# Optimization experiments

Hardware: AMD Instinct MI355X
Metric: run time of the kernel (lower is better)

The kernel has to match this reference:

```python
import jax, jax.numpy as jnp
import numpy as np

B, N, DIM = 4, 2048, 512
HEADS, DK = 8, 64
SCALE = DK ** -0.5


def setup_inputs() -> dict:
    key = jax.random.key(0)
    k1, k2, k3, k4 = jax.random.split(key, 4)
    x = jax.random.normal(k1, (B, N, DIM), dtype=jnp.float32)
    # nn.Linear(dim, dim_key*heads, bias=False): y = x @ W.T; store W already transposed
    Wq = jax.random.normal(k2, (DIM, HEADS * DK), dtype=jnp.float32) * (DIM ** -0.5)
    Wk = jax.random.normal(k3, (DIM, HEADS * DK), dtype=jnp.float32) * (DIM ** -0.5)
    rel_content_bias = jax.random.normal(k4, (1, HEADS, 1, DK), dtype=jnp.float32)
    return {"x": x, "Wq": Wq, "Wk": Wk, "rel_content_bias": rel_content_bias}


def _split_heads(t, h):
    # [b, n, h*d] -> [b, h, n, d]
    b, n, hd = t.shape
    return t.reshape(b, n, h, hd // h).transpose(0, 2, 1, 3)


def reference(x, Wq, Wk, rel_content_bias):
    q = _split_heads(x @ Wq, HEADS) * SCALE          # [b, h, n, dk]
    k = _split_heads(x @ Wk, HEADS)                  # [b, h, n, dk]
    v = _split_heads(x, HEADS)                       # [b, h, n, dim/h]
    logits = jnp.einsum('bhid,bhjd->bhij', q + rel_content_bias, k)
    attn = jax.nn.sigmoid(logits)                    # no softmax normalization
    out = jnp.einsum('bhij,bhjd->bhid', attn, v)     # [b, h, n, dim/h]
    b, h, n, d = out.shape
    return out.transpose(0, 2, 1, 3).reshape(b, n, h * d)
```

## Files before the change

kernel.cpp:

```cpp
#include <hip/hip_runtime.h>
#include <hip/hip_bf16.h>
#include <stdint.h>

#define BB 4
#define NN 2048
#define DIMD 512
#define HH 8
#define DKK 64
#define MTOT (BB * NN)
constexpr float SCALE = 0.125f;
constexpr float L2E = 1.44269504089f;

typedef __attribute__((ext_vector_type(4))) float f32x4;
typedef __attribute__((ext_vector_type(2))) float f32x2;
typedef __attribute__((ext_vector_type(8))) short bf16x8;
typedef __attribute__((ext_vector_type(4))) _Float16 f16x4;
typedef __attribute__((ext_vector_type(2))) __fp16 fp16v2;
typedef __attribute__((ext_vector_type(4))) __fp16 fp16v4;
typedef __attribute__((ext_vector_type(2))) unsigned int u32x2;

union pack8 { unsigned short s[8]; uint4 v; };
union fragu { u32x2 h[2]; bf16x8 v; };

__device__ __forceinline__ unsigned short f2bf(float f) {
  union { float f; uint32_t u; } v; v.f = f;
  uint32_t u = v.u;
  return (unsigned short)((u + 0x7FFFu + ((u >> 16) & 1u)) >> 16);
}

__device__ __forceinline__ unsigned short f2h(float f) {
  union { _Float16 h; unsigned short u; } c; c.h = (_Float16)f;
  return c.u;
}

__device__ __forceinline__ bf16x8 ld_frag(const unsigned short* p) {
  fragu f;
  f.h[0] = *(const u32x2*)p;
  f.h[1] = *(const u32x2*)(p + 4);
  return f.v;
}
__device__ __forceinline__ void st8(unsigned short* p, uint4 v) {
  *(u32x2*)p = (u32x2){v.x, v.y};
  *(u32x2*)(p + 4) = (u32x2){v.z, v.w};
}

__device__ __forceinline__ f16x4 sig_pack(f32x4 sv) {
  float e0 = __builtin_amdgcn_exp2f(-__builtin_fabsf(sv[0]));
  float e1 = __builtin_amdgcn_exp2f(-__builtin_fabsf(sv[1]));
  float e2 = __builtin_amdgcn_exp2f(-__builtin_fabsf(sv[2]));
  float e3 = __builtin_amdgcn_exp2f(-__builtin_fabsf(sv[3]));
  const f32x2 c3 = {-0.22184f, -0.22184f};
  const f32x2 c2 = {0.66550f, 0.66550f};
  const f32x2 c1 = {-0.94280f, -0.94280f};
  const f32x2 c0 = {0.49826f, 0.49826f};
  f32x2 eA = {e0, e1}, eB = {e2, e3};
  f32x2 pA = __builtin_elementwise_fma(
      __builtin_elementwise_fma(__builtin_elementwise_fma(c3, eA, c2), eA, c1),
      eA, c0);
  f32x2 pB = __builtin_elementwise_fma(
      __builtin_elementwise_fma(__builtin_elementwise_fma(c3, eB, c2), eB, c1),
      eB, c0);
  float r0 = __builtin_copysignf(pA.x, sv[0]);
  float r1 = __builtin_copysignf(pA.y, sv[1]);
  float r2 = __builtin_copysignf(pB.x, sv[2]);
  float r3 = __builtin_copysignf(pB.y, sv[3]);
  fp16v2 lo = __builtin_amdgcn_cvt_pkrtz(r0, r1);
  fp16v2 hi = __builtin_amdgcn_cvt_pkrtz(r2, r3);
  fp16v4 p;
  p.x = lo.x; p.y = lo.y; p.z = hi.x; p.w = hi.y;
  return __builtin_bit_cast(f16x4, p);
}

__global__ __launch_bounds__(256) void prep(const float* __restrict__ x,
                                            const float* __restrict__ wq,
                                            const float* __restrict__ wk,
                                            unsigned short* __restrict__ xtf,
                                            unsigned short* __restrict__ wtq,
                                            unsigned short* __restrict__ wtk,
                                            float* __restrict__ vsum_p) {
  const int bx = blockIdx.x, tid = threadIdx.x;
  if (bx < 256) {
    __shared__ float Pred[4][64];
    int q = bx;
    int b = q >> 6, r = q & 63;
    int dt = r >> 3, nt = r & 7;
    int dl = tid & 63, c = tid >> 6;
    int d = dt * 64 + dl;
    int n0 = nt * 256 + c * 64;
    const float* xp = x + ((size_t)b * NN + n0) * DIMD + d;
    unsigned short* dp = xtf + ((size_t)b * DIMD + d) * NN + n0;
    float s = 0.f;
#pragma unroll
    for (int g = 0; g < 8; g++) {
      pack8 pa;
#pragma unroll
      for (int k = 0; k < 8; k++) {
        float v = xp[(size_t)(g * 8 + k) * DIMD];
        s += v;
        pa.s[k] = f2h(v);
      }
      *(uint4*)(dp + g * 8) = pa.v;
    }
    Pred[c][dl] = s;
    __syncthreads();
    if (c == 0) {
      float t = Pred[0][dl] + Pred[1][dl] + Pred[2][dl] + Pred[3][dl];
      vsum_p[((size_t)b * 8 + nt) * DIMD + d] = t;
    }
  } else {
    __shared__ __align__(16) unsigned short T[64][68];
    int q = bx - 256;
    const float* w = (q >= 64) ? wk : wq;
    unsigned short* wt = (q >= 64) ? wtk : wtq;
    int r = q & 63;
    int kt = r >> 3, nt = r & 7;
    const int k0 = kt * 64, n0 = nt * 64;
#pragma unroll
    for (int rr = 0; rr < 16; rr++) {
      int idx = tid + rr * 256;
      int kl = idx >> 6, nl = idx & 63;
      T[nl][kl] = f2bf(w[(size_t)(k0 + kl) * DIMD + n0 + nl]);
    }
    __syncthreads();
#pragma unroll
    for (int rr = 0; rr < 2; rr++) {
      int idx = tid + rr * 256;
      int nl = idx >> 3, c = idx & 7;
      fragu f;
      f.h[0] = *(const u32x2*)&T[nl][c * 8];
      f.h[1] = *(const u32x2*)&T[nl][c * 8 + 4];
      uint4 v;
      v.x = f.h[0].x; v.y = f.h[0].y; v.z = f.h[1].x; v.w = f.h[1].y;
      *(uint4*)(wt + (size_t)(n0 + nl) * DIMD + k0 + c * 8) = v;
    }
  }
}

__global__ __launch_bounds__(512, 4) void qk_gemm(const float* __restrict__ x,
                                                  const unsigned short* __restrict__ wtq,
                                                  const unsigned short* __restrict__ wtk,
                                                  const float* __restrict__ bias,
                                                  unsigned short* __restrict__ qout,
                                                  unsigned short* __restrict__ kout) {
  __shared__ __align__(16) unsigned short Als[128][68];
  __shared__ __align__(16) unsigned short Bls[128][68];
  const int mb = blockIdx.x, nb = blockIdx.y;
  const bool isQ = (nb < 4);
  const unsigned short* wt = isQ ? wtq : wtk;
  unsigned short* outp = isQ ? qout : kout;
  const int n0 = (nb & 3) * 128, m0 = mb * 128;
  const int tid = threadIdx.x;
  const int wave = tid >> 6, lane = tid & 63;
  const int quad = lane >> 4, l16 = lane & 15;
  const int wm = wave >> 2, wn = wave & 3;

  f32x4 acc[4][2];
#pragma unroll
  for (int a = 0; a < 4; a++)
#pragma unroll
    for (int c = 0; c < 2; c++) acc[a][c] = (f32x4){0.f, 0.f, 0.f, 0.f};

  const int srow[2] = {tid >> 3, (tid + 512) >> 3};
  const int scol = (tid & 7) * 8;
  uint4 pa[2], pb[2];

  auto loadA = [&](int r, int k0) -> uint4 {
    const float* ap = x + (size_t)(m0 + srow[r]) * DIMD + k0 + scol;
    float4 a = *(const float4*)ap;
    float4 b = *(const float4*)(ap + 4);
    pack8 p;
    p.s[0] = f2bf(a.x); p.s[1] = f2bf(a.y); p.s[2] = f2bf(a.z); p.s[3] = f2bf(a.w);
    p.s[4] = f2bf(b.x); p.s[5] = f2bf(b.y); p.s[6] = f2bf(b.z); p.s[7] = f2bf(b.w);
    return p.v;
  };

#pragma unroll
  for (int r = 0; r < 2; r++) {
    pa[r] = loadA(r, 0);
    pb[r] = *(const uint4*)(wt + (size_t)(n0 + srow[r]) * DIMD + scol);
  }

  for (int k0 = 0; k0 < DIMD; k0 += 64) {
    __syncthreads();
#pragma unroll
    for (int r = 0; r < 2; r++) {
      st8(&Als[srow[r]][scol], pa[r]);
      st8(&Bls[srow[r]][scol], pb[r]);
    }
    __syncthreads();
    if (k0 + 64 < DIMD) {
#pragma unroll
      for (int r = 0; r < 2; r++) {
        pa[r] = loadA(r, k0 + 64);
        pb[r] = *(const uint4*)(wt + (size_t)(n0 + srow[r]) * DIMD + k0 + 64 + scol);
      }
    }
#pragma unroll
    for (int ks = 0; ks < 2; ks++) {
      bf16x8 af[4], bfr[2];
#pragma unroll
      for (int t = 0; t < 4; t++)
        af[t] = ld_frag(&Als[wm * 64 + t * 16 + l16][quad * 8 + ks * 32]);
#pragma unroll
      for (int t = 0; t < 2; t++)
        bfr[t] = ld_frag(&Bls[wn * 32 + t * 16 + l16][quad * 8 + ks * 32]);
#pragma unroll
      for (int tm = 0; tm < 4; tm++)
#pragma unroll
        for (int tn = 0; tn < 2; tn++)
          acc[tm][tn] =
              __builtin_amdgcn_mfma_f32_16x16x32_bf16(af[tm], bfr[tn], acc[tm][tn], 0, 0, 0);
    }
  }
#pragma unroll
  for (int tm = 0; tm < 4; tm++) {
#pragma unroll
    for (int tn = 0; tn < 2; tn++) {
      int gcol = n0 + wn * 32 + tn * 16 + l16;
      float bl = isQ ? bias[gcol] * L2E : 0.f;
#pragma unroll
      for (int r = 0; r < 4; r++) {
        int row = m0 + wm * 64 + tm * 16 + quad * 4 + r;
        float v = acc[tm][tn][r];
        if (isQ) v = v * (SCALE * L2E) + bl;
        outp[(size_t)row * DIMD + gcol] = f2bf(v);
      }
    }
  }
}

__global__ __launch_bounds__(512, 4) void attn(const unsigned short* __restrict__ qb,
                                               const unsigned short* __restrict__ kb,
                                               const unsigned short* __restrict__ xtf,
                                               const float* __restrict__ vsum_p,
                                               float* __restrict__ out) {
  __shared__ __align__(16) char smem[34816];
  unsigned short* Kall = (unsigned short*)smem;
  unsigned short* Vall = Kall + 2 * 64 * 68;
  float* R0 = (float*)smem;

  const int bh = blockIdx.x, it = blockIdx.y;
  const int b = bh >> 3, h = bh & 7;
  const int i0 = it * 128;
  const int tid = threadIdx.x;
  const int lane = tid & 63;
  const int grp = tid >> 8;
  const int wv = (tid >> 6) & 3;
  const int gtid = tid & 255;
  const int quad = lane >> 4, l16 = lane & 15;

  bf16x8 qf[2][2];
  int irow[2];
#pragma unroll
  for (int s_ = 0; s_ < 2; s_++) {
    irow[s_] = i0 + wv * 32 + s_ * 16 + l16;
    const unsigned short* qp = qb + ((size_t)b * NN + irow[s_]) * DIMD + h * DKK + quad * 8;
    qf[s_][0] = *(const bf16x8*)qp;
    qf[s_][1] = *(const bf16x8*)(qp + 32);
  }

  f32x4 o[2][4];
#pragma unroll
  for (int s_ = 0; s_ < 2; s_++)
#pragma unroll
    for (int td = 0; td < 4; td++) o[s_][td] = (f32x4){0.f, 0.f, 0.f, 0.f};

  const unsigned short* kbase = kb + (size_t)b * NN * DIMD + h * DKK;
  const unsigned short* vbase = xtf + ((size_t)b * DIMD + h * DKK) * NN;
  unsigned short* Kg = Kall + grp * (64 * 68);
  unsigned short* Vg = Vall + grp * (64 * 68);
  const int jbase = grp * 1024;

  const int trow[2] = {gtid >> 3, (gtid + 256) >> 3};
  const int tcol = (gtid & 7) * 8;
  uint4 pk[2], pv[2];
#pragma unroll
  for (int r = 0; r < 2; r++) {
    pk[r] = *(const uint4*)(kbase + (size_t)(jbase + trow[r]) * DIMD + tcol);
    pv[r] = *(const uint4*)(vbase + (size_t)trow[r] * NN + jbase + tcol);
  }

  for (int itr = 0; itr < 16; itr++) {
    __syncthreads();
#pragma unroll
    for (int r = 0; r < 2; r++) {
      st8(&Kg[trow[r] * 68 + tcol], pk[r]);
      st8(&Vg[trow[r] * 68 + tcol], pv[r]);
    }
    __syncthreads();
    if (itr < 15) {
      const int j0 = jbase + (itr + 1) * 64;
#pragma unroll
      for (int r = 0; r < 2; r++) {
        pk[r] = *(const uint4*)(kbase + (size_t)(j0 + trow[r]) * DIMD + tcol);
        pv[r] = *(const uint4*)(vbase + (size_t)trow[r] * NN + j0 + tcol);
      }
    }

    __builtin_amdgcn_s_setprio(1);
#pragma unroll
    for (int t = 0; t < 4; t++) {
      bf16x8 kf0 = ld_frag(&Kg[(t * 16 + l16) * 68 + quad * 8]);
      bf16x8 kf1 = ld_frag(&Kg[(t * 16 + l16) * 68 + quad * 8 + 32]);
      f16x4 pf[2];
#pragma unroll
      for (int s_ = 0; s_ < 2; s_++) {
        f32x4 sv = (f32x4){0.f, 0.f, 0.f, 0.f};
        sv = __builtin_amdgcn_mfma_f32_16x16x32_bf16(kf0, qf[s_][0], sv, 0, 0, 0);
        sv = __builtin_amdgcn_mfma_f32_16x16x32_bf16(kf1, qf[s_][1], sv, 0, 0, 0);
        pf[s_] = sig_pack(sv);
      }
#pragma unroll
      for (int td = 0; td < 4; td++) {
        f16x4 vf = __builtin_bit_cast(
            f16x4, *(const u32x2*)&Vg[(td * 16 + l16) * 68 + t * 16 + quad * 4]);
        o[0][td] = __builtin_amdgcn_mfma_f32_16x16x16f16(vf, pf[0], o[0][td], 0, 0, 0);
        o[1][td] = __builtin_amdgcn_mfma_f32_16x16x16f16(vf, pf[1], o[1][td], 0, 0, 0);
      }
    }
    __builtin_amdgcn_s_setprio(0);
  }

  __syncthreads();
  if (grp == 1) {
#pragma unroll
    for (int s_ = 0; s_ < 2; s_++)
#pragma unroll
      for (int td = 0; td < 4; td++) {
        int base = (wv * 32 + s_ * 16 + l16) * 66 + td * 16 + quad * 4;
        *(f32x2*)&R0[base] = (f32x2){o[s_][td][0], o[s_][td][1]};
        *(f32x2*)&R0[base + 2] = (f32x2){o[s_][td][2], o[s_][td][3]};
      }
  }
  __syncthreads();
  if (grp == 0) {
    const float* vp = vsum_p + (size_t)b * 8 * DIMD + h * DKK;
    f32x4 vs[4];
#pragma unroll
    for (int td = 0; td < 4; td++) {
      f32x4 a = (f32x4){0.f, 0.f, 0.f, 0.f};
#pragma unroll
      for (int p = 0; p < 8; p++) {
        f32x4 t = *(const f32x4*)&vp[(size_t)p * DIMD + td * 16 + quad * 4];
        a[0] += t[0]; a[1] += t[1]; a[2] += t[2]; a[3] += t[3];
      }
      vs[td] = a;
    }
#pragma unroll
    for (int s_ = 0; s_ < 2; s_++) {
#pragma unroll
      for (int td = 0; td < 4; td++) {
        int base = (wv * 32 + s_ * 16 + l16) * 66 + td * 16 + quad * 4;
        f32x2 a = *(const f32x2*)&R0[base];
        f32x2 c = *(const f32x2*)&R0[base + 2];
        o[s_][td][0] += a.x + 0.5f * vs[td][0];
        o[s_][td][1] += a.y + 0.5f * vs[td][1];
        o[s_][td][2] += c.x + 0.5f * vs[td][2];
        o[s_][td][3] += c.y + 0.5f * vs[td][3];
        float* op = out + ((size_t)b * NN + irow[s_]) * DIMD + h * DKK + td * 16 + quad * 4;
        *(f32x4*)op = o[s_][td];
      }
    }
  }
}

extern "C" void kernel_launch(void* const* d_in, const int* in_sizes, int n_in,
                              void* d_out, int out_size, void* d_ws, size_t ws_size,
                              hipStream_t stream) {
  const float* x = (const float*)d_in[0];
  const float* Wq = (const float*)d_in[1];
  const float* Wk = (const float*)d_in[2];
  const float* bias = (const float*)d_in[3];
  float* out = (float*)d_out;

  unsigned short* ws = (unsigned short*)d_ws;
  unsigned short* xtf = ws;
  unsigned short* wtq = xtf + (size_t)MTOT * DIMD;
  unsigned short* wtk = wtq + (size_t)DIMD * DIMD;
  unsigned short* qb = wtk + (size_t)DIMD * DIMD;
  unsigned short* kb = qb + (size_t)MTOT * DIMD;
  float* vsum_p = (float*)(kb + (size_t)MTOT * DIMD);

  prep<<<dim3(384), 256, 0, stream>>>(x, Wq, Wk, xtf, wtq, wtk, vsum_p);
  qk_gemm<<<dim3(64, 8), 512, 0, stream>>>(x, wtq, wtk, bias, qb, kb);
  attn<<<dim3(32, 16), 512, 0, stream>>>(qb, kb, xtf, vsum_p, out);
}
```

Before: 150.3 us.

## Use 16x16x32 f16 MFMA for PV with permuted K layout and 128-key tiles

Doubles the key tile per iteration from 64 to 128, halving the number of barrier-synchronised iterations, and replaces the 16x16x16 f16 MFMA in the P*V product with the 16x16x32 variant. K rows are stored in shared memory through a bit permutation, so two 16-key score tiles concatenate directly into the 8-element operand layout the wider MFMA expects. This cuts MFMA instruction count and sync overhead. In exchange, shared memory per block roughly doubles, which may reduce occupancy at 512 threads per block, and more prefetch registers are held live.

After: 154.2 us. +2.6%, slower.

```diff
diff --git a/kernel.cpp b/kernel.cpp
--- a/kernel.cpp
+++ b/kernel.cpp
@@ -15,12 +15,14 @@
 typedef __attribute__((ext_vector_type(2))) float f32x2;
 typedef __attribute__((ext_vector_type(8))) short bf16x8;
 typedef __attribute__((ext_vector_type(4))) _Float16 f16x4;
+typedef __attribute__((ext_vector_type(8))) _Float16 f16x8;
 typedef __attribute__((ext_vector_type(2))) __fp16 fp16v2;
 typedef __attribute__((ext_vector_type(4))) __fp16 fp16v4;
 typedef __attribute__((ext_vector_type(2))) unsigned int u32x2;
 
 union pack8 { unsigned short s[8]; uint4 v; };
 union fragu { u32x2 h[2]; bf16x8 v; };
+union cat8u { f16x4 h[2]; f16x8 v; };
 
 __device__ __forceinline__ unsigned short f2bf(float f) {
   union { float f; uint32_t u; } v; v.f = f;
@@ -42,6 +44,14 @@
 __device__ __forceinline__ void st8(unsigned short* p, uint4 v) {
   *(u32x2*)p = (u32x2){v.x, v.y};
   *(u32x2*)(p + 4) = (u32x2){v.z, v.w};
+}
+
+__device__ __forceinline__ f16x8 cat8(f16x4 a, f16x4 b) {
+  cat8u u; u.h[0] = a; u.h[1] = b; return u.v;
+}
+
+__device__ __forceinline__ int kperm(int j) {
+  return (j & 96) | ((j & 4) << 2) | ((j & 24) >> 1) | (j & 3);
 }
 
 __device__ __forceinline__ f16x4 sig_pack(f32x4 sv) {
@@ -234,9 +244,9 @@
                                                const unsigned short* __restrict__ xtf,
                                                const float* __restrict__ vsum_p,
                                                float* __restrict__ out) {
-  __shared__ __align__(16) char smem[34816];
+  __shared__ __align__(16) char smem[68608];
   unsigned short* Kall = (unsigned short*)smem;
-  unsigned short* Vall = Kall + 2 * 64 * 68;
+  unsigned short* Vall = Kall + 2 * 128 * 68;
   float* R0 = (float*)smem;
 
   const int bh = blockIdx.x, it = blockIdx.y;
@@ -267,55 +277,58 @@
 
   const unsigned short* kbase = kb + (size_t)b * NN * DIMD + h * DKK;
   const unsigned short* vbase = xtf + ((size_t)b * DIMD + h * DKK) * NN;
-  unsigned short* Kg = Kall + grp * (64 * 68);
-  unsigned short* Vg = Vall + grp * (64 * 68);
+  unsigned short* Kg = Kall + grp * (128 * 68);
+  unsigned short* Vg = Vall + grp * (64 * 132);
   const int jbase = grp * 1024;
 
-  const int trow[2] = {gtid >> 3, (gtid + 256) >> 3};
-  const int tcol = (gtid & 7) * 8;
-  uint4 pk[2], pv[2];
-#pragma unroll
-  for (int r = 0; r < 2; r++) {
-    pk[r] = *(const uint4*)(kbase + (size_t)(jbase + trow[r]) * DIMD + tcol);
-    pv[r] = *(const uint4*)(vbase + (size_t)trow[r] * NN + jbase + tcol);
-  }
-
-  for (int itr = 0; itr < 16; itr++) {
-    __syncthreads();
-#pragma unroll
-    for (int r = 0; r < 2; r++) {
-      st8(&Kg[trow[r] * 68 + tcol], pk[r]);
-      st8(&Vg[trow[r] * 68 + tcol], pv[r]);
-    }
-    __syncthreads();
-    if (itr < 15) {
-      const int j0 = jbase + (itr + 1) * 64;
-#pragma unroll
-      for (int r = 0; r < 2; r++) {
-        pk[r] = *(const uint4*)(kbase + (size_t)(j0 + trow[r]) * DIMD + tcol);
-        pv[r] = *(const uint4*)(vbase + (size_t)trow[r] * NN + j0 + tcol);
-      }
-    }
+  const int krow = gtid >> 3, kcol = (gtid & 7) * 8;
+  const int vrow = gtid >> 4, vcol = (gtid & 15) * 8;
+  uint4 pk[4], pv[4];
+
+  auto prefetch = [&](int t) {
+    const int jb = jbase + t * 128;
+#pragma unroll
+    for (int r = 0; r < 4; r++) {
+      pk[r] = *(const uint4*)(kbase + (size_t)(jb + krow + 32 * r) * DIMD + kcol);
+      pv[r] = *(const uint4*)(vbase + (size_t)(vrow + 16 * r) * NN + jb + vcol);
+    }
+  };
+  prefetch(0);
+
+  for (int itr = 0; itr < 8; itr++) {
+    __syncthreads();
+#pragma unroll
+    for (int r = 0; r < 4; r++) {
+      st8(&Kg[kperm(krow + 32 * r) * 68 + kcol], pk[r]);
+      st8(&Vg[(vrow + 16 * r) * 132 + vcol], pv[r]);
+    }
+    __syncthreads();
+    if (itr < 7) prefetch(itr + 1);
 
     __builtin_amdgcn_s_setprio(1);
 #pragma unroll
-    for (int t = 0; t < 4; t++) {
-      bf16x8 kf0 = ld_frag(&Kg[(t * 16 + l16) * 68 + quad * 8]);
-      bf16x8 kf1 = ld_frag(&Kg[(t * 16 + l16) * 68 + quad * 8 + 32]);
-      f16x4 pf[2];
+    for (int a = 0; a < 4; a++) {
+      bf16x8 ke0 = ld_frag(&Kg[((2 * a) * 16 + l16) * 68 + quad * 8]);
+      bf16x8 ke1 = ld_frag(&Kg[((2 * a) * 16 + l16) * 68 + quad * 8 + 32]);
+      bf16x8 ko0 = ld_frag(&Kg[((2 * a + 1) * 16 + l16) * 68 + quad * 8]);
+      bf16x8 ko1 = ld_frag(&Kg[((2 * a + 1) * 16 + l16) * 68 + quad * 8 + 32]);
+      f16x8 pf[2];
 #pragma unroll
       for (int s_ = 0; s_ < 2; s_++) {
-        f32x4 sv = (f32x4){0.f, 0.f, 0.f, 0.f};
-        sv = __builtin_amdgcn_mfma_f32_16x16x32_bf16(kf0, qf[s_][0], sv, 0, 0, 0);
-        sv = __builtin_amdgcn_mfma_f32_16x16x32_bf16(kf1, qf[s_][1], sv, 0, 0, 0);
-        pf[s_] = sig_pack(sv);
+        f32x4 se = (f32x4){0.f, 0.f, 0.f, 0.f};
+        f32x4 so = (f32x4){0.f, 0.f, 0.f, 0.f};
+        se = __builtin_amdgcn_mfma_f32_16x16x32_bf16(ke0, qf[s_][0], se, 0, 0, 0);
+        se = __builtin_amdgcn_mfma_f32_16x16x32_bf16(ke1, qf[s_][1], se, 0, 0, 0);
+        so = __builtin_amdgcn_mfma_f32_16x16x32_bf16(ko0, qf[s_][0], so, 0, 0, 0);
+        so = __builtin_amdgcn_mfma_f32_16x16x32_bf16(ko1, qf[s_][1], so, 0, 0, 0);
+        pf[s_] = cat8(sig_pack(se), sig_pack(so));
       }
 #pragma unroll
       for (int td = 0; td < 4; td++) {
-        f16x4 vf = __builtin_bit_cast(
-            f16x4, *(const u32x2*)&Vg[(td * 16 + l16) * 68 + t * 16 + quad * 4]);
-        o[0][td] = __builtin_amdgcn_mfma_f32_16x16x16f16(vf, pf[0], o[0][td], 0, 0, 0);
-        o[1][td] = __builtin_amdgcn_mfma_f32_16x16x16f16(vf, pf[1], o[1][td], 0, 0, 0);
+        f16x8 vf = __builtin_bit_cast(
+            f16x8, ld_frag(&Vg[(td * 16 + l16) * 132 + a * 32 + quad * 8]));
+        o[0][td] = __builtin_amdgcn_mfma_f32_16x16x32_f16(vf, pf[0], o[0][td], 0, 0, 0);
+        o[1][td] = __builtin_amdgcn_mfma_f32_16x16x32_f16(vf, pf[1], o[1][td], 0, 0, 0);
       }
     }
     __builtin_amdgcn_s_setprio(0);
```
